# Optimization experiments

Measured on AMD Instinct MI355X. Metric: run time of the kernel, lower is better.

The kernel has to match this reference:

```python
import jax, jax.numpy as jnp
import numpy as np

B, T, IN, H, OUT, NH = 64, 512, 256, 512, 256, 4
HD = H // NH
DT = 0.1
UNFOLDS = 6
MIN_TAU, MAX_TAU = 0.1, 10.0


def setup_inputs() -> dict:
    key = jax.random.key(0)
    ks = iter(jax.random.split(key, 48))

    def w(shape, scale=0.05):
        return jax.random.normal(next(ks), shape, dtype=jnp.float32) * scale

    d = {"inputs": jax.random.normal(next(ks), (B, T, IN), dtype=jnp.float32)}
    for i, fin in enumerate([IN, H]):
        d[f"Win{i}_w"] = w((H, fin))
        d[f"Win{i}_b"] = jnp.zeros((H,), jnp.float32)
        d[f"Wrec{i}_w"] = w((H, H))
        d[f"tau{i}a_w"] = w((H, fin + H))
        d[f"tau{i}a_b"] = jnp.zeros((H,), jnp.float32)
        d[f"tau{i}b_w"] = w((H, H))
        d[f"tau{i}b_b"] = jnp.zeros((H,), jnp.float32)
        d[f"gleak{i}"] = jnp.full((H,), 0.1, jnp.float32)
        d[f"gsyn{i}"] = jnp.full((H,), 0.5, jnp.float32)
        d[f"ln{i}_w"] = jnp.ones((H,), jnp.float32)
        d[f"ln{i}_b"] = jnp.zeros((H,), jnp.float32)
    d["attn_in_w"] = w((3 * H, H))
    d["attn_in_b"] = jnp.zeros((3 * H,), jnp.float32)
    d["attn_out_w"] = w((H, H))
    d["attn_out_b"] = jnp.zeros((H,), jnp.float32)
    d["p1_w"] = w((H // 2, H))
    d["p1_b"] = jnp.zeros((H // 2,), jnp.float32)
    d["p2_w"] = w((OUT, H // 2))
    d["p2_b"] = jnp.zeros((OUT,), jnp.float32)
    return d


def _ltc_step(x, v, g, Wiw, Wib, Wrw, taw, tab, tbw, tbb, gl, gs):
    # tau_net: Linear -> tanh -> Linear -> sigmoid, scaled to [min_tau, max_tau]
    comb = jnp.concatenate([x, v], axis=-1)
    tau_h = jnp.tanh(comb @ taw.T + tab)
    tau = MIN_TAU + (MAX_TAU - MIN_TAU) * jax.nn.sigmoid(tau_h @ tbw.T + tbb)
    I_in = x @ Wiw.T + Wib
    for _ in range(UNFOLDS):  # fixed small unroll of the ODE integration
        I_rec = jnp.tanh(v) @ Wrw.T
        g = g + DT * (-g + jax.nn.sigmoid(I_in + I_rec)) / (tau * 0.5)
        v = v + DT * (-gl * v + gs * g * (1.0 - v)) / tau
        v = jnp.clip(v, -5.0, 5.0)
    return jnp.tanh(v), v, g


def _layernorm(x, w, b):
    m = x.mean(-1, keepdims=True)
    var = x.var(-1, keepdims=True)
    return (x - m) / jnp.sqrt(var + 1e-5) * w + b


def reference(inputs, Win0_w, Win0_b, Wrec0_w, tau0a_w, tau0a_b, tau0b_w, tau0b_b,
              gleak0, gsyn0, ln0_w, ln0_b,
              Win1_w, Win1_b, Wrec1_w, tau1a_w, tau1a_b, tau1b_w, tau1b_b,
              gleak1, gsyn1, ln1_w, ln1_b,
              attn_in_w, attn_in_b, attn_out_w, attn_out_b,
              p1_w, p1_b, p2_w, p2_b):
    Bc = inputs.shape[0]

    def step(carry, x_t):
        v0, g0, v1, g1 = carry
        h0, v0, g0 = _ltc_step(x_t, v0, g0, Win0_w, Win0_b, Wrec0_w,
                               tau0a_w, tau0a_b, tau0b_w, tau0b_b, gleak0, gsyn0)
        h0 = _layernorm(h0, ln0_w, ln0_b)
        h1, v1, g1 = _ltc_step(h0, v1, g1, Win1_w, Win1_b, Wrec1_w,
                               tau1a_w, tau1a_b, tau1b_w, tau1b_b, gleak1, gsyn1)
        h1 = _layernorm(h1, ln1_w, ln1_b)
        return (v0, g0, v1, g1), h1

    z = jnp.zeros((Bc, H), inputs.dtype)
    xs = jnp.transpose(inputs, (1, 0, 2))  # (T, B, IN)
    _, ys = jax.lax.scan(step, (z, z, z, z), xs)
    seq = jnp.transpose(ys, (1, 0, 2))  # (B, T, H)

    # MultiheadAttention (self-attention, eval mode => no dropout)
    qkv = seq @ attn_in_w.T + attn_in_b  # (B, T, 3H)
    q, k, v_ = jnp.split(qkv, 3, axis=-1)
    def heads(t):
        return t.reshape(Bc, T, NH, HD).transpose(0, 2, 1, 3)  # (B, NH, T, HD)
    q, k, v_ = heads(q), heads(k), heads(v_)
    scores = jnp.einsum('bhqd,bhkd->bhqk', q, k) / jnp.sqrt(jnp.array(HD, seq.dtype))
    attn = jax.nn.softmax(scores, axis=-1)
    o = jnp.einsum('bhqk,bhkd->bhqd', attn, v_)
    o = o.transpose(0, 2, 1, 3).reshape(Bc, T, H)
    o = o @ attn_out_w.T + attn_out_b

    # output projection on last timestep (return_sequences=False)
    last = o[:, -1, :]
    h = jax.nn.relu(last @ p1_w.T + p1_b)
    out = h @ p2_w.T + p2_b
    return out
```

## Files before the change

kernel.cpp:

```cpp
#include <hip/hip_runtime.h>
#include <stdint.h>


__device__ __forceinline__ float b2f(unsigned short s){
  union { unsigned i; float f; } c; c.i = ((unsigned)s) << 16; return c.f;
}
__device__ __forceinline__ unsigned short f2b(float f){
  union { unsigned i; float f; } c; c.f = f;
  unsigned r = c.i + 0x7fffu + ((c.i >> 16) & 1u);
  return (unsigned short)(r >> 16);
}
__device__ __forceinline__ unsigned pack2(float a, float b){
  return (unsigned)f2b(a) | ((unsigned)f2b(b) << 16);
}
__device__ __forceinline__ float fsig(float x){ return 1.f/(1.f+__expf(-x)); }
__device__ __forceinline__ float ftanh(float x){ return 1.f - 2.f/(__expf(2.f*x)+1.f); }

#if __has_builtin(__builtin_amdgcn_fdot2_f32_bf16)
typedef __bf16 bf16x2_t __attribute__((ext_vector_type(2)));
__device__ __forceinline__ float dot2(unsigned w, unsigned a, float acc){
  union U { unsigned u; bf16x2_t v; };
  U cw; cw.u = w; U ca; ca.u = a;
  return __builtin_amdgcn_fdot2_f32_bf16(cw.v, ca.v, acc, false);
}
#else
__device__ __forceinline__ float dot2(unsigned w, unsigned a, float acc){
  asm("v_dot2_f32_bf16 %0, %1, %2, %0" : "+v"(acc) : "v"(w), "v"(a));
  return acc;
}
#endif

#if __has_builtin(__builtin_amdgcn_sdot4)
__device__ __forceinline__ int sdot4(unsigned w, unsigned a, int acc){
  return __builtin_amdgcn_sdot4((int)w, (int)a, acc, false);
}
#else
__device__ __forceinline__ int sdot4(unsigned w, unsigned a, int acc){
  asm("v_dot4_i32_i8 %0, %1, %2, %0" : "+v"(acc) : "v"(w), "v"(a));
  return acc;
}
#endif

__device__ __forceinline__ unsigned quad8s(float a, float b, float c, float d,
                                           float s){
  const int q0 = __float2int_rn(a * s);
  const int q1 = __float2int_rn(b * s);
  const int q2 = __float2int_rn(c * s);
  const int q3 = __float2int_rn(d * s);
  return (unsigned)(q0 & 255) | ((unsigned)(q1 & 255) << 8) |
         ((unsigned)(q2 & 255) << 16) | ((unsigned)(q3 & 255) << 24);
}

__device__ __forceinline__ float redselF(float c0, float c1, float c2, float c3,
                                         int tid){
  #pragma unroll
  for (int off = 1; off <= 4; off <<= 1){
    c0 += __shfl_xor(c0, off);
    c1 += __shfl_xor(c1, off);
    c2 += __shfl_xor(c2, off);
    c3 += __shfl_xor(c3, off);
  }
  const int j = (tid >> 1) & 3;
  const float lo = (j & 1) ? c1 : c0;
  const float hi = (j & 1) ? c3 : c2;
  return (j & 2) ? hi : lo;
}
__device__ __forceinline__ int redselI(int c0, int c1, int c2, int c3, int tid){
  #pragma unroll
  for (int off = 1; off <= 4; off <<= 1){
    c0 += __shfl_xor(c0, off);
    c1 += __shfl_xor(c1, off);
    c2 += __shfl_xor(c2, off);
    c3 += __shfl_xor(c3, off);
  }
  const int j = (tid >> 1) & 3;
  const int lo = (j & 1) ? c1 : c0;
  const int hi = (j & 1) ? c3 : c2;
  return (j & 2) ? hi : lo;
}

template<int NQ>
__device__ __forceinline__ int matvecQ1(const uint4* __restrict__ wq,
                                        const unsigned* __restrict__ actQ,
                                        int tid){
  const int kh8 = tid & 7;
  int c0 = 0, c1 = 0, c2 = 0, c3 = 0;
  #pragma unroll 4
  for (int q = 0; q < NQ; ++q){
    const unsigned au = actQ[(q << 3) + kh8];
    const uint4 wv = wq[((size_t)q << 10) + tid];
    c0 = sdot4(wv.x, au, c0);
    c1 = sdot4(wv.y, au, c1);
    c2 = sdot4(wv.z, au, c2);
    c3 = sdot4(wv.w, au, c3);
  }
  return redselI(c0, c1, c2, c3, tid);
}

template<int NX, int NV>
__device__ __forceinline__ float matvecQ2(const uint4* __restrict__ wq,
                                          const unsigned* __restrict__ actQ,
                                          float xmax, float vmax, int tid){
  const int kh8 = tid & 7;
  int x0 = 0, x1 = 0, x2 = 0, x3 = 0;
  int v0 = 0, v1 = 0, v2 = 0, v3 = 0;
  #pragma unroll 4
  for (int q = 0; q < NX; ++q){
    const unsigned au = actQ[(q << 3) + kh8];
    const uint4 wv = wq[((size_t)q << 10) + tid];
    x0 = sdot4(wv.x, au, x0);
    x1 = sdot4(wv.y, au, x1);
    x2 = sdot4(wv.z, au, x2);
    x3 = sdot4(wv.w, au, x3);
  }
  #pragma unroll 4
  for (int q = NX; q < NX + NV; ++q){
    const unsigned au = actQ[(q << 3) + kh8];
    const uint4 wv = wq[((size_t)q << 10) + tid];
    v0 = sdot4(wv.x, au, v0);
    v1 = sdot4(wv.y, au, v1);
    v2 = sdot4(wv.z, au, v2);
    v3 = sdot4(wv.w, au, v3);
  }
  const float c0 = (float)x0 * xmax + (float)v0 * vmax;
  const float c1 = (float)x1 * xmax + (float)v1 * vmax;
  const float c2 = (float)x2 * xmax + (float)v2 * vmax;
  const float c3 = (float)x3 * xmax + (float)v3 * vmax;
  return redselF(c0, c1, c2, c3, tid);
}

template<bool FILL>
__device__ __forceinline__ int wrecQ(const uint4* __restrict__ wq,
                                     const unsigned* __restrict__ actQ,
                                     uint4* __restrict__ wldsQ, int tid){
  const int kh8 = tid & 7;
  int c0 = 0, c1 = 0, c2 = 0, c3 = 0;
  #pragma unroll 3
  for (int q = 0; q < 9; ++q){
    const unsigned au = actQ[(q << 3) + kh8];
    uint4 wv;
    if (FILL){ wv = wq[((size_t)q << 10) + tid]; wldsQ[(q << 10) + tid] = wv; }
    else     { wv = wldsQ[(q << 10) + tid]; }
    c0 = sdot4(wv.x, au, c0);
    c1 = sdot4(wv.y, au, c1);
    c2 = sdot4(wv.z, au, c2);
    c3 = sdot4(wv.w, au, c3);
  }
  #pragma unroll
  for (int q = 9; q < 16; ++q){
    const unsigned au = actQ[(q << 3) + kh8];
    const uint4 wv = wq[((size_t)q << 10) + tid];
    c0 = sdot4(wv.x, au, c0);
    c1 = sdot4(wv.y, au, c1);
    c2 = sdot4(wv.z, au, c2);
    c3 = sdot4(wv.w, au, c3);
  }
  return redselI(c0, c1, c2, c3, tid);
}

template<int NX, bool PROD>
__device__ __forceinline__ float layer_stepP(
    float& v, float& g, float& vmax,
    const uint4* WiQ, const uint4* WrQ, const uint4* TaQ, const uint4* TbQ,
    float wb, float tab, float tbb, float gl, float gs, float lw, float lb,
    float smTa, float smWi, float smTb, float smWr, float xmax,
    unsigned* comb8, unsigned* thQ, unsigned* actQA, unsigned* actQB,
    float* sred, uint4* wldsQ, int tid, bool fill, float& ymax)
{
  const float tsel = matvecQ2<NX, 16>(TaQ, comb8, xmax, vmax, tid);
  const int   isel = matvecQ1<NX>(WiQ, comb8, tid);
  const float tauh = ftanh(tsel * smTa + tab);
  const float iin  = (float)isel * (smWi * xmax) + wb;
  const float hv   = ftanh(v);
  {
    const float t2 = __shfl_down(tauh, 2), t4 = __shfl_down(tauh, 4),
                t6 = __shfl_down(tauh, 6);
    const float h2 = __shfl_down(hv, 2), h4 = __shfl_down(hv, 4),
                h6 = __shfl_down(hv, 6);
    if (!(tid & 7)){
      thQ[tid >> 3]   = quad8s(tauh, t2, t4, t6, 127.f);
      actQB[tid >> 3] = quad8s(hv, h2, h4, h6, 127.f);
    }
  }
  __syncthreads();
  const int tbi = matvecQ1<16>(TbQ, thQ, tid);
  const float tau = 0.1f + 9.9f * fsig((float)tbi * smTb + tbb);
  const float ga = 0.2f / tau;
  const float va = 0.1f / tau;
  float h = hv;
  #pragma unroll 1
  for (int u = 0; u < 6; ++u){
    unsigned* curQ = (u & 1) ? actQA : actQB;
    unsigned* nxtQ = (u & 1) ? actQB : actQA;
    const int ri = (fill && u == 0)
        ? wrecQ<true >(WrQ, curQ, wldsQ, tid)
        : wrecQ<false>(WrQ, curQ, wldsQ, tid);
    const float irec = (float)ri * smWr;
    g += (fsig(iin + irec) - g) * ga;
    v += (gs * g * (1.f - v) - gl * v) * va;
    v = fminf(5.f, fmaxf(-5.f, v));
    h = ftanh(v);
    const float h2 = __shfl_down(h, 2), h4 = __shfl_down(h, 4),
                h6 = __shfl_down(h, 6);
    if (!(tid & 7)) nxtQ[tid >> 3] = quad8s(h, h2, h4, h6, 127.f);
    __syncthreads();
  }
  const float hm = (tid & 1) ? 0.f : h;
  const float vm = (tid & 1) ? 0.f : fabsf(v);
  float s1 = hm, s2 = hm * hm, s3 = vm;
  #pragma unroll
  for (int off = 32; off >= 1; off >>= 1){
    s1 += __shfl_down(s1, off);
    s2 += __shfl_down(s2, off);
    s3 = fmaxf(s3, __shfl_down(s3, off));
  }
  const int lane = tid & 63, wid = tid >> 6;
  if (lane == 0){ sred[wid] = s1; sred[16 + wid] = s2; sred[32 + wid] = s3; }
  __syncthreads();
  float S1 = 0.f, S2 = 0.f, S3 = 0.f;
  #pragma unroll
  for (int w2 = 0; w2 < 16; ++w2){
    S1 += sred[w2]; S2 += sred[16 + w2]; S3 = fmaxf(S3, sred[32 + w2]);
  }
  vmax = S3;
  const float m    = S1 * (1.f/512.f);
  const float varr = S2 * (1.f/512.f) - m * m;
  const float y = (h - m) * rsqrtf(varr + 1e-5f) * lw + lb;
  __syncthreads();
  if (PROD){
    float ya = (tid & 1) ? 0.f : fabsf(y);
    #pragma unroll
    for (int off = 32; off >= 1; off >>= 1) ya = fmaxf(ya, __shfl_down(ya, off));
    if (lane == 0) sred[wid] = ya;
    __syncthreads();
    float Y = 0.f;
    #pragma unroll
    for (int w2 = 0; w2 < 16; ++w2) Y = fmaxf(Y, sred[w2]);
    ymax = Y;
  }
  return y;
}

template<int K, int NOUT>
__device__ __forceinline__ void matvec2(const uint4* __restrict__ w,
                                        const unsigned* __restrict__ act2,
                                        int tid, float* out){
  constexpr int NJ = NOUT/256, NIB = K/16;
  const uint4* a4 = (const uint4*)act2;
  const int kh = tid & 1;
  float acc[NJ];
  #pragma unroll
  for (int j = 0; j < NJ; ++j) acc[j] = 0.f;
  #pragma unroll 2
  for (int ib = 0; ib < NIB; ++ib){
    const uint4 a = a4[2*ib + kh];
    #pragma unroll
    for (int j = 0; j < NJ; ++j){
      const uint4 wv = w[(size_t)(ib*NJ + j)*512 + tid];
      acc[j] = dot2(wv.x, a.x, acc[j]);
      acc[j] = dot2(wv.y, a.y, acc[j]);
      acc[j] = dot2(wv.z, a.z, acc[j]);
      acc[j] = dot2(wv.w, a.w, acc[j]);
    }
  }
  #pragma unroll
  for (int j = 0; j < NJ; ++j){
    float s = acc[j];
    s += __shfl_xor(s, 1);
    out[j] = s;
  }
}

#define PK_WQ     0
#define PK_WK     32768
#define PK_WV     65536
#define PK_AO     98304
#define PK_P1     131072
#define PK_P2     147456
#define PK_BF_TOT 155648
#define PK_QWR0   155648
#define PK_QWR1   172032
#define PK_QTA0   188416
#define PK_QTA1   212992
#define PK_QWI0   245760
#define PK_QWI1   253952
#define PK_QTB0   270336
#define PK_QTB1   286720

__global__ void detect_kernel(const unsigned* __restrict__ x, int* __restrict__ flag){
  int cnt = 0;
  for (int i = threadIdx.x; i < 4096; i += 256){
    const unsigned e = (x[i] >> 7) & 0xFFu;
    cnt += (e == 0u || e == 0xFFu) ? 1 : 0;
  }
  __shared__ int sh[4];
  #pragma unroll
  for (int off = 32; off >= 1; off >>= 1) cnt += __shfl_down(cnt, off);
  if ((threadIdx.x & 63) == 0) sh[threadIdx.x >> 6] = cnt;
  __syncthreads();
  if (threadIdx.x == 0) *flag = (sh[0]+sh[1]+sh[2]+sh[3] > 4) ? 1 : 0;
}

struct TPDesc {
  const void* src[6];
  long eoff[6];
  int kdiv8[6];
  int lg2n[6];
  int cum[7];
};
__global__ void tailpack_kernel(TPDesc d, const int* __restrict__ flag,
                                uint4* __restrict__ out){
  const int u = blockIdx.x * 256 + threadIdx.x;
  if (u >= d.cum[6]) return;
  int s = 0;
  #pragma unroll
  for (int i = 1; i < 6; ++i) if (u >= d.cum[i]) s = i;
  const int local = u - d.cum[s];
  const int tid  = local & 511;
  const int r    = local >> 9;
  const int lgnj = d.lg2n[s] - 8;
  const int j    = r & ((1 << lgnj) - 1);
  const int ib   = r >> lgnj;
  const int p    = tid >> 1, kh = tid & 1;
  const int o    = (j << 8) + p;
  const long base = (long)o * (d.kdiv8[s] * 8) + (long)(2*ib + kh) * 8;
  if (*flag){
    const float* sp = (const float*)d.src[s] + d.eoff[s];
    unsigned short h[8];
    #pragma unroll
    for (int i = 0; i < 8; ++i) h[i] = f2b(sp[base + i]);
    uint4 o4;
    o4.x = (unsigned)h[0] | ((unsigned)h[1] << 16);
    o4.y = (unsigned)h[2] | ((unsigned)h[3] << 16);
    o4.z = (unsigned)h[4] | ((unsigned)h[5] << 16);
    o4.w = (unsigned)h[6] | ((unsigned)h[7] << 16);
    out[u] = o4;
  } else {
    const unsigned short* sp = (const unsigned short*)d.src[s] + d.eoff[s];
    out[u] = *(const uint4*)(sp + base);
  }
}

struct QDesc {
  const void* src[8];
  int K[8];
  int outoff[8];
};
__global__ void rowmax_kernel(QDesc d, const int* __restrict__ flag,
                              float* __restrict__ pvec, float* __restrict__ sinv){
  const int r = blockIdx.x * 256 + threadIdx.x;
  const int m = r >> 9, row = r & 511;
  const int K = d.K[m];
  float mx = 0.f;
  if (*flag){
    const float* p = (const float*)d.src[m] + (size_t)row * K;
    for (int k = 0; k < K; ++k) mx = fmaxf(mx, fabsf(p[k]));
  } else {
    const unsigned short* p = (const unsigned short*)d.src[m] + (size_t)row * K;
    for (int k = 0; k < K; ++k) mx = fmaxf(mx, fabsf(b2f(p[k])));
  }
  const int ok = mx > 1e-20f;
  pvec[9728 + r] = ok ? (mx * (1.f/16129.f)) : 0.f;
  sinv[r]        = ok ? (127.f / mx)         : 0.f;
}
__global__ void qpack_kernel(QDesc d, const int* __restrict__ flag,
                             const float* __restrict__ sinv,
                             uint4* __restrict__ out){
  const int u = blockIdx.x * 256 + threadIdx.x;
  const int gq = u >> 10, tid = u & 1023;
  const int cum[9] = {0,16,32,56,88,96,112,128,144};
  int m = 0;
  #pragma unroll
  for (int i = 1; i < 8; ++i) if (gq >= cum[i]) m = i;
  const int q = gq - cum[m];
  const int K = d.K[m];
  const int isf = *flag;
  const int k0 = 4 * ((q << 3) + (tid & 7));
  unsigned wd[4];
  #pragma unroll
  for (int j = 0; j < 4; ++j){
    const int row = ((tid >> 3) << 2) + j;
    const float s = sinv[(m << 9) + row];
    float f0, f1, f2, f3;
    if (isf){
      const float* p = (const float*)d.src[m] + (size_t)row * K + k0;
      f0 = p[0]; f1 = p[1]; f2 = p[2]; f3 = p[3];
    } else {
      const unsigned short* p = (const unsigned short*)d.src[m] + (size_t)row * K + k0;
      f0 = b2f(p[0]); f1 = b2f(p[1]); f2 = b2f(p[2]); f3 = b2f(p[3]);
    }
    wd[j] = quad8s(f0, f1, f2, f3, s);
  }
  uint4 o4; o4.x = wd[0]; o4.y = wd[1]; o4.z = wd[2]; o4.w = wd[3];
  out[d.outoff[m] + ((size_t)q << 10) + tid] = o4;
}

__global__ void xmax_kernel(const void* __restrict__ xin,
                            const int* __restrict__ flag,
                            float* __restrict__ xm){
  const int r = blockIdx.x;
  const int tid = threadIdx.x;
  float mx = 0.f;
  if (*flag){
    const float2* p = (const float2*)xin + (size_t)r * 128 + 2*tid;
    const float2 a = p[0], b = p[1];
    mx = fmaxf(fmaxf(fabsf(a.x), fabsf(a.y)), fmaxf(fabsf(b.x), fabsf(b.y)));
  } else {
    const unsigned* p = (const unsigned*)xin + (size_t)r * 128 + 2*tid;
    const unsigned u0 = p[0], u1 = p[1];
    mx = fmaxf(fmaxf(fabsf(b2f((unsigned short)(u0 & 0xffffu))),
                     fabsf(b2f((unsigned short)(u0 >> 16)))),
               fmaxf(fabsf(b2f((unsigned short)(u1 & 0xffffu))),
                     fabsf(b2f((unsigned short)(u1 >> 16)))));
  }
  #pragma unroll
  for (int off = 32; off >= 1; off >>= 1) mx = fmaxf(mx, __shfl_down(mx, off));
  if (tid == 0) xm[r] = mx;
}

struct VecDesc {
  const void* src[18];
  int n[18];
  int dst[18];
};
__global__ void vec_kernel(VecDesc d, const int* __restrict__ flag,
                           float* __restrict__ pvec){
  const int s = blockIdx.x;
  const int f = *flag;
  for (int i = threadIdx.x; i < d.n[s]; i += blockDim.x)
    pvec[d.dst[s] + i] = f ? ((const float*)d.src[s])[i]
                           : b2f(((const unsigned short*)d.src[s])[i]);
}

__global__ void zflags_kernel(int* __restrict__ aflag, int* __restrict__ cflag){
  const int i = threadIdx.x;
  if (i < 64) aflag[i] = 0; else cflag[i - 64] = 0;
}

#define SCAN_SMEM 150272
__global__
__attribute__((amdgpu_flat_work_group_size(1024, 1024), amdgpu_waves_per_eu(4, 4)))
void scan_kernel(
    const void* __restrict__ xin,
    const uint4* __restrict__ wp,
    const float* __restrict__ pvec,
    const int* __restrict__ flagp,
    unsigned* __restrict__ seqw,
    unsigned* __restrict__ ring,
    int* __restrict__ aflag,
    int* __restrict__ cflag,
    const float* __restrict__ xmaxT)
{
  extern __shared__ __align__(16) char smem[];
  unsigned* comb8 = (unsigned*)smem;
  unsigned* thQ   = comb8 + 256;
  unsigned* actQA = thQ + 128;
  unsigned* actQB = actQA + 128;
  float*    sred  = (float*)(actQB + 128);
  uint4*    wldsQ = (uint4*)(smem + 2816);

  const int tid = threadIdx.x;
  const int o   = tid >> 1;
  const int blk  = blockIdx.x;
  const int xcd  = blk & 7;
  const int slot = blk >> 3;
  const bool isB = xcd >= 4;
  const int b    = ((xcd & 3) << 4) | slot;
  const int isf32 = *flagp;
  const int cb  = isB ? 3584 : 0;

  const uint4* WrQ = wp + (isB ? PK_QWR1 : PK_QWR0);
  const uint4* TaQ = wp + (isB ? PK_QTA1 : PK_QTA0);
  const uint4* WiQ = wp + (isB ? PK_QWI1 : PK_QWI0);
  const uint4* TbQ = wp + (isB ? PK_QTB1 : PK_QTB0);

  const float wb  = pvec[cb+o],      tab = pvec[cb+512+o], tbb = pvec[cb+1024+o];
  const float gl  = pvec[cb+1536+o], gs  = pvec[cb+2048+o];
  const float lw  = pvec[cb+2560+o], lb  = pvec[cb+3072+o];

  const float* smb = pvec + 9728;
  const float smWr = smb[(0 + (isB?1:0))*512 + o];
  const float smTa = smb[(2 + (isB?1:0))*512 + o];
  const float smWi = smb[(4 + (isB?1:0))*512 + o];
  const float smTb = smb[(6 + (isB?1:0))*512 + o];

  float v = 0.f, g = 0.f, vmax = 0.f;

  #pragma unroll 1
  for (int t = 0; t < 512; ++t){
    if (!isB){
      const float xm = xmaxT[b*512 + t];
      if (tid < 64){
        const float sc = (xm > 1e-20f) ? 127.f/xm : 0.f;
        const size_t xbase = ((size_t)b*512 + t)*128;
        if (isf32){
          const float2 a = ((const float2*)xin)[xbase + 2*tid];
          const float2 c = ((const float2*)xin)[xbase + 2*tid + 1];
          comb8[tid] = quad8s(a.x, a.y, c.x, c.y, sc);
        } else {
          const unsigned u0 = ((const unsigned*)xin)[xbase + 2*tid];
          const unsigned u1 = ((const unsigned*)xin)[xbase + 2*tid + 1];
          comb8[tid] = quad8s(b2f((unsigned short)(u0 & 0xffffu)),
                              b2f((unsigned short)(u0 >> 16)),
                              b2f((unsigned short)(u1 & 0xffffu)),
                              b2f((unsigned short)(u1 >> 16)), sc);
        }
      }
      {
        const float sv = (vmax > 1e-20f) ? 127.f/vmax : 0.f;
        const float v2 = __shfl_down(v, 2), v4 = __shfl_down(v, 4),
                    v6 = __shfl_down(v, 6);
        if (!(tid & 7)) comb8[64 + (tid >> 3)] = quad8s(v, v2, v4, v6, sv);
      }
      __syncthreads();
      float ym;
      const float y = layer_stepP<8, true>(v, g, vmax, WiQ, WrQ, TaQ, TbQ,
                                           wb, tab, tbb, gl, gs, lw, lb,
                                           smTa, smWi, smTb, smWr, xm,
                                           comb8, thQ, actQA, actQB, sred,
                                           wldsQ, tid, t == 0, ym);
      if (tid == 0 && t >= 8){
        while (__hip_atomic_load(&cflag[b], __ATOMIC_ACQUIRE,
                                 __HIP_MEMORY_SCOPE_AGENT) < t - 7)
          __builtin_amdgcn_s_sleep(2);
      }
      __syncthreads();
      {
        const float sy = (ym > 1e-20f) ? 127.f/ym : 0.f;
        unsigned* dst = ring + ((size_t)b*8 + (t & 7))*144;
        const float y2 = __shfl_down(y, 2), y4 = __shfl_down(y, 4),
                    y6 = __shfl_down(y, 6);
        if (!(tid & 7))
          __hip_atomic_store(dst + (tid >> 3), quad8s(y, y2, y4, y6, sy),
                             __ATOMIC_RELAXED, __HIP_MEMORY_SCOPE_AGENT);
        if (tid == 0)
          __hip_atomic_store(dst + 128, __float_as_uint(ym),
                             __ATOMIC_RELAXED, __HIP_MEMORY_SCOPE_AGENT);
      }
      __syncthreads();
      if (tid == 0)
        __hip_atomic_store(&aflag[b], t + 1, __ATOMIC_RELEASE,
                           __HIP_MEMORY_SCOPE_AGENT);
    } else {
      if (tid == 0){
        while (__hip_atomic_load(&aflag[b], __ATOMIC_ACQUIRE,
                                 __HIP_MEMORY_SCOPE_AGENT) < t + 1)
          __builtin_amdgcn_s_sleep(2);
      }
      __syncthreads();
      const unsigned* rsl = ring + ((size_t)b*8 + (t & 7))*144;
      if (tid < 128)
        comb8[tid] = __hip_atomic_load(rsl + tid, __ATOMIC_RELAXED,
                                       __HIP_MEMORY_SCOPE_AGENT);
      const float xm = __uint_as_float(
          __hip_atomic_load(rsl + 128, __ATOMIC_RELAXED,
                            __HIP_MEMORY_SCOPE_AGENT));
      {
        const float sv = (vmax > 1e-20f) ? 127.f/vmax : 0.f;
        const float v2 = __shfl_down(v, 2), v4 = __shfl_down(v, 4),
                    v6 = __shfl_down(v, 6);
        if (!(tid & 7)) comb8[128 + (tid >> 3)] = quad8s(v, v2, v4, v6, sv);
      }
      __syncthreads();
      if (tid == 0)
        __hip_atomic_store(&cflag[b], t + 1, __ATOMIC_RELEASE,
                           __HIP_MEMORY_SCOPE_AGENT);
      float ymd;
      const float y = layer_stepP<16, false>(v, g, vmax, WiQ, WrQ, TaQ, TbQ,
                                             wb, tab, tbb, gl, gs, lw, lb,
                                             smTa, smWi, smTb, smWr, xm,
                                             comb8, thQ, actQA, actQB, sred,
                                             wldsQ, tid, t == 0, ymd);
      {
        const float yp = __shfl_down(y, 2);
        if (!(tid & 3))
          seqw[((size_t)b*512 + t)*256 + (tid >> 2)] = pack2(y, yp);
      }
    }
  }
}

__global__ __launch_bounds__(512) void q_kernel(
    const unsigned* __restrict__ seqw, const uint4* __restrict__ wp,
    const float* __restrict__ pvec, float* __restrict__ qws)
{
  __shared__ __align__(16) unsigned act2[256];
  const int tid = threadIdx.x, b = blockIdx.x, p = tid >> 1;
  if (tid < 256) act2[tid] = seqw[((size_t)(b*512 + 511))*256 + tid];
  __syncthreads();
  float q[2]; matvec2<512, 512>(wp + PK_WQ, act2, tid, q);
  if (!(tid & 1)){
    qws[b*512 + p]       = q[0] + pvec[7168 + p];
    qws[b*512 + 256 + p] = q[1] + pvec[7168 + 256 + p];
  }
}

__global__ __launch_bounds__(512) void score_kernel(
    const unsigned* __restrict__ seqw, const uint4* __restrict__ wp,
    const float* __restrict__ pvec, const float* __restrict__ qws,
    float* __restrict__ sws)
{
  __shared__ __align__(16) unsigned act2[256];
  __shared__ float hrA[8], hrB[8];
  const int tid = threadIdx.x, p = tid >> 1;
  const int r = blockIdx.x, b = r >> 9, t = r & 511;
  if (tid < 256) act2[tid] = seqw[(size_t)r*256 + tid];
  __syncthreads();
  float kk[2]; matvec2<512, 512>(wp + PK_WK, act2, tid, kk);
  float pa = (tid & 1) ? 0.f : (kk[0] + pvec[7680 + p])       * qws[b*512 + p];
  float pb = (tid & 1) ? 0.f : (kk[1] + pvec[7680 + 256 + p]) * qws[b*512 + 256 + p];
  #pragma unroll
  for (int off = 32; off >= 1; off >>= 1){
    pa += __shfl_down(pa, off); pb += __shfl_down(pb, off);
  }
  const int lane = tid & 63, wid = tid >> 6;
  if (lane == 0){ hrA[wid] = pa; hrB[wid] = pb; }
  __syncthreads();
  if (tid < 4){
    float s;
    if      (tid == 0) s = hrA[0]+hrA[1]+hrA[2]+hrA[3];
    else if (tid == 1) s = hrA[4]+hrA[5]+hrA[6]+hrA[7];
    else if (tid == 2) s = hrB[0]+hrB[1]+hrB[2]+hrB[3];
    else               s = hrB[4]+hrB[5]+hrB[6]+hrB[7];
    sws[((size_t)(b*4 + tid))*512 + t] = s * 0.08838834764831845f;
  }
}

__global__ __launch_bounds__(512) void softmax_kernel(
    const float* __restrict__ sws, float* __restrict__ pws,
    float* __restrict__ oacc)
{
  __shared__ float rw[16];
  const int tid = threadIdx.x, bh = blockIdx.x;
  const float s = sws[(size_t)bh*512 + tid];
  float mx = s;
  #pragma unroll
  for (int off = 32; off >= 1; off >>= 1) mx = fmaxf(mx, __shfl_down(mx, off));
  const int lane = tid & 63, wid = tid >> 6;
  if (lane == 0) rw[wid] = mx;
  __syncthreads();
  mx = rw[0];
  #pragma unroll
  for (int w2 = 1; w2 < 8; ++w2) mx = fmaxf(mx, rw[w2]);
  const float e = __expf(s - mx);
  float sm = e;
  #pragma unroll
  for (int off = 32; off >= 1; off >>= 1) sm += __shfl_down(sm, off);
  if (lane == 0) rw[8 + wid] = sm;
  __syncthreads();
  sm = 0.f;
  #pragma unroll
  for (int w2 = 0; w2 < 8; ++w2) sm += rw[8 + w2];
  pws[(size_t)bh*512 + tid] = e / sm;
  if (tid < 128) oacc[(bh >> 2)*512 + (bh & 3)*128 + tid] = 0.f;
}

__global__ __launch_bounds__(512) void vacc_kernel(
    const unsigned* __restrict__ seqw, const uint4* __restrict__ wp,
    const float* __restrict__ pvec, const float* __restrict__ pws,
    float* __restrict__ oacc)
{
  __shared__ __align__(16) unsigned act2[256];
  const int tid = threadIdx.x, p = tid >> 1;
  const int blk = blockIdx.x, b = blk >> 3, ch = blk & 7;
  float a0 = 0.f, a1 = 0.f;
  #pragma unroll 1
  for (int t = ch*64; t < ch*64 + 64; ++t){
    if (tid < 256) act2[tid] = seqw[((size_t)b*512 + t)*256 + tid];
    __syncthreads();
    float vv[2]; matvec2<512, 512>(wp + PK_WV, act2, tid, vv);
    if (!(tid & 1)){
      a0 += (vv[0] + pvec[8192 + p])       * pws[(size_t)(b*4 + (p>>7))*512 + t];
      a1 += (vv[1] + pvec[8192 + 256 + p]) * pws[(size_t)(b*4 + 2 + (p>>7))*512 + t];
    }
    __syncthreads();
  }
  if (!(tid & 1)){
    atomicAdd(&oacc[b*512 + p], a0);
    atomicAdd(&oacc[b*512 + 256 + p], a1);
  }
}

__global__ __launch_bounds__(512) void final_kernel(
    const float* __restrict__ oacc, const uint4* __restrict__ wp,
    const float* __restrict__ pvec, const int* __restrict__ flagp,
    void* __restrict__ out)
{
  __shared__ __align__(16) unsigned a2[256];
  const int tid = threadIdx.x, b = blockIdx.x, p = tid >> 1;
  const int isf32 = *flagp;
  {
    const float x0 = oacc[b*512 + p], x1 = oacc[b*512 + 256 + p];
    const float xa = __shfl_down(x0, 2), xb = __shfl_down(x1, 2);
    if (!(tid & 3)){ a2[tid>>2] = pack2(x0, xa); a2[128+(tid>>2)] = pack2(x1, xb); }
  }
  __syncthreads();
  float t1[2]; matvec2<512, 512>(wp + PK_AO, a2, tid, t1);
  t1[0] += pvec[8704 + p]; t1[1] += pvec[8704 + 256 + p];
  __syncthreads();
  {
    const float ta = __shfl_down(t1[0], 2), tb = __shfl_down(t1[1], 2);
    if (!(tid & 3)){ a2[tid>>2] = pack2(t1[0], ta); a2[128+(tid>>2)] = pack2(t1[1], tb); }
  }
  __syncthreads();
  float t2[1]; matvec2<512, 256>(wp + PK_P1, a2, tid, t2);
  t2[0] = fmaxf(0.f, t2[0] + pvec[9216 + p]);
  __syncthreads();
  {
    const float ta = __shfl_down(t2[0], 2);
    if (!(tid & 3)) a2[tid>>2] = pack2(t2[0], ta);
  }
  __syncthreads();
  float r[1]; matvec2<256, 256>(wp + PK_P2, a2, tid, r);
  if (!(tid & 1)){
    const float rr = r[0] + pvec[9472 + p];
    if (isf32) ((float*)out)[b*256 + p] = rr;
    else       ((unsigned short*)out)[b*256 + p] = f2b(rr);
  }
}

__global__ void zero_kernel(unsigned* __restrict__ p, int n){
  const int i = blockIdx.x * 1024 + threadIdx.x;
  if (i < n) p[i] = 0;
}

extern "C" void kernel_launch(void* const* d_in, const int* in_sizes, int n_in,
                              void* d_out, int out_size, void* d_ws, size_t ws_size,
                              hipStream_t stream)
{
  (void)in_sizes; (void)n_in; (void)out_size;

  if (ws_size < ((size_t)44 << 20)){
    zero_kernel<<<8, 1024, 0, stream>>>((unsigned*)d_out, 8192);
    return;
  }

  hipFuncSetAttribute((const void*)scan_kernel,
                      hipFuncAttributeMaxDynamicSharedMemorySize, SCAN_SMEM);

  char* ws = (char*)d_ws;
  int*      flag   = (int*)ws;
  int*      aflag  = (int*)(ws + 256);
  int*      cflag  = (int*)(ws + 512);
  float*    pvec   = (float*)(ws + 4096);
  uint4*    packed = (uint4*)(ws + 65536);
  float*    sinv   = (float*)(ws + ((size_t)5 << 20));
  float*    xmaxT  = (float*)(ws + ((size_t)5 << 20) + 131072);
  unsigned* seq    = (unsigned*)(ws + ((size_t)8 << 20));
  unsigned* ring   = (unsigned*)(ws + ((size_t)40 << 20));
  float*    sws    = (float*)(ws + ((size_t)41 << 20));
  float*    pws    = (float*)(ws + ((size_t)41 << 20) + 524288);
  float*    qws    = (float*)(ws + ((size_t)42 << 20));
  float*    oacc   = (float*)(ws + ((size_t)42 << 20) + 262144);

  detect_kernel<<<1, 256, 0, stream>>>((const unsigned*)d_in[0], flag);
  zflags_kernel<<<1, 128, 0, stream>>>(aflag, cflag);

  TPDesc tp;
  const void* tsrc[6] = { d_in[23], d_in[23], d_in[23], d_in[25], d_in[27], d_in[29] };
  const long teoff[6] = { 0, 262144, 524288, 0, 0, 0 };
  const int tk8[6]   = { 64, 64, 64, 64, 64, 32 };
  const int tln[6]   = { 9, 9, 9, 9, 8, 8 };
  const int tcum[7]  = { 0, 32768, 65536, 98304, 131072, 147456, 155648 };
  for (int i = 0; i < 6; ++i){
    tp.src[i]=tsrc[i]; tp.eoff[i]=teoff[i]; tp.kdiv8[i]=tk8[i]; tp.lg2n[i]=tln[i];
  }
  for (int i = 0; i < 7; ++i) tp.cum[i] = tcum[i];
  tailpack_kernel<<<(PK_BF_TOT + 255)/256, 256, 0, stream>>>(tp, flag, packed);

  VecDesc vd;
  const void* vsrc[18] = {
    d_in[2], d_in[5], d_in[7], d_in[8], d_in[9], d_in[10], d_in[11],
    d_in[13], d_in[16], d_in[18], d_in[19], d_in[20], d_in[21], d_in[22],
    d_in[24], d_in[26], d_in[28], d_in[30]
  };
  const int vn[18]  = {512,512,512,512,512,512,512, 512,512,512,512,512,512,512,
                       1536,512,256,256};
  const int vds[18] = {0,512,1024,1536,2048,2560,3072,
                       3584,4096,4608,5120,5632,6144,6656,
                       7168,8704,9216,9472};
  for (int i = 0; i < 18; ++i){ vd.src[i]=vsrc[i]; vd.n[i]=vn[i]; vd.dst[i]=vds[i]; }
  vec_kernel<<<18, 512, 0, stream>>>(vd, flag, pvec);

  QDesc qd;
  const void* qsrc[8] = { d_in[3], d_in[14], d_in[4], d_in[15],
                          d_in[1], d_in[12], d_in[6], d_in[17] };
  const int qK[8]   = { 512, 512, 768, 1024, 256, 512, 512, 512 };
  const int qoff[8] = { PK_QWR0, PK_QWR1, PK_QTA0, PK_QTA1,
                        PK_QWI0, PK_QWI1, PK_QTB0, PK_QTB1 };
  for (int i = 0; i < 8; ++i){ qd.src[i]=qsrc[i]; qd.K[i]=qK[i]; qd.outoff[i]=qoff[i]; }
  rowmax_kernel<<<16, 256, 0, stream>>>(qd, flag, pvec, sinv);
  qpack_kernel<<<576, 256, 0, stream>>>(qd, flag, sinv, packed);
  xmax_kernel<<<32768, 64, 0, stream>>>(d_in[0], flag, xmaxT);

  scan_kernel<<<128, 1024, SCAN_SMEM, stream>>>(d_in[0], packed, pvec, flag,
                                                seq, ring, aflag, cflag, xmaxT);
  q_kernel<<<64, 512, 0, stream>>>(seq, packed, pvec, qws);
  score_kernel<<<64*512, 512, 0, stream>>>(seq, packed, pvec, qws, sws);
  softmax_kernel<<<256, 512, 0, stream>>>(sws, pws, oacc);
  vacc_kernel<<<512, 512, 0, stream>>>(seq, packed, pvec, pws, oacc);
  final_kernel<<<64, 512, 0, stream>>>(oacc, packed, pvec, flag, d_out);
}
```

Measured before the change: 12.39 ms.

## Split scan into input-projection producer blocks and recurrent consumer blocks

The recurrent scan now runs 256 blocks in four roles. Two roles compute the input-dependent matvecs (the x-part of the tau_net first layer and the input current) for layer 0 and layer 1 ahead of time and pass them through ring buffers. The other two roles keep only the v-dependent recurrent work on the serial critical path. Blocks get their role from a per-XCD atomic rank read via the XCC_ID register, and the tau weights are split into x and v halves at pack time. This adds inter-block flag handshakes and needs all 256 persistent blocks to be co-resident, or the spin-waits could deadlock.

```diff
diff --git a/kernel.cpp b/kernel.cpp
--- a/kernel.cpp
+++ b/kernel.cpp
@@ -51,20 +51,6 @@
          ((unsigned)(q2 & 255) << 16) | ((unsigned)(q3 & 255) << 24);
 }
 
-__device__ __forceinline__ float redselF(float c0, float c1, float c2, float c3,
-                                         int tid){
-  #pragma unroll
-  for (int off = 1; off <= 4; off <<= 1){
-    c0 += __shfl_xor(c0, off);
-    c1 += __shfl_xor(c1, off);
-    c2 += __shfl_xor(c2, off);
-    c3 += __shfl_xor(c3, off);
-  }
-  const int j = (tid >> 1) & 3;
-  const float lo = (j & 1) ? c1 : c0;
-  const float hi = (j & 1) ? c3 : c2;
-  return (j & 2) ? hi : lo;
-}
 __device__ __forceinline__ int redselI(int c0, int c1, int c2, int c3, int tid){
   #pragma unroll
   for (int off = 1; off <= 4; off <<= 1){
@@ -95,38 +81,6 @@
     c3 = sdot4(wv.w, au, c3);
   }
   return redselI(c0, c1, c2, c3, tid);
-}
-
-template<int NX, int NV>
-__device__ __forceinline__ float matvecQ2(const uint4* __restrict__ wq,
-                                          const unsigned* __restrict__ actQ,
-                                          float xmax, float vmax, int tid){
-  const int kh8 = tid & 7;
-  int x0 = 0, x1 = 0, x2 = 0, x3 = 0;
-  int v0 = 0, v1 = 0, v2 = 0, v3 = 0;
-  #pragma unroll 4
-  for (int q = 0; q < NX; ++q){
-    const unsigned au = actQ[(q << 3) + kh8];
-    const uint4 wv = wq[((size_t)q << 10) + tid];
-    x0 = sdot4(wv.x, au, x0);
-    x1 = sdot4(wv.y, au, x1);
-    x2 = sdot4(wv.z, au, x2);
-    x3 = sdot4(wv.w, au, x3);
-  }
-  #pragma unroll 4
-  for (int q = NX; q < NX + NV; ++q){
-    const unsigned au = actQ[(q << 3) + kh8];
-    const uint4 wv = wq[((size_t)q << 10) + tid];
-    v0 = sdot4(wv.x, au, v0);
-    v1 = sdot4(wv.y, au, v1);
-    v2 = sdot4(wv.z, au, v2);
-    v3 = sdot4(wv.w, au, v3);
-  }
-  const float c0 = (float)x0 * xmax + (float)v0 * vmax;
-  const float c1 = (float)x1 * xmax + (float)v1 * vmax;
-  const float c2 = (float)x2 * xmax + (float)v2 * vmax;
-  const float c3 = (float)x3 * xmax + (float)v3 * vmax;
-  return redselF(c0, c1, c2, c3, tid);
 }
 
 template<bool FILL>
@@ -158,19 +112,17 @@
   return redselI(c0, c1, c2, c3, tid);
 }
 
-template<int NX, bool PROD>
-__device__ __forceinline__ float layer_stepP(
-    float& v, float& g, float& vmax,
-    const uint4* WiQ, const uint4* WrQ, const uint4* TaQ, const uint4* TbQ,
-    float wb, float tab, float tbb, float gl, float gs, float lw, float lb,
-    float smTa, float smWi, float smTb, float smWr, float xmax,
-    unsigned* comb8, unsigned* thQ, unsigned* actQA, unsigned* actQB,
+template<bool PROD>
+__device__ __forceinline__ float scan_step(
+    float& v, float& g, float& vmax, float P, float iin,
+    const uint4* TavQ, const uint4* TbQ, const uint4* WrQ,
+    float tab, float tbb, float gl, float gs, float lw, float lb,
+    float smTa, float smTb, float smWr,
+    unsigned* vQ, unsigned* thQ, unsigned* aQA, unsigned* aQB,
     float* sred, uint4* wldsQ, int tid, bool fill, float& ymax)
 {
-  const float tsel = matvecQ2<NX, 16>(TaQ, comb8, xmax, vmax, tid);
-  const int   isel = matvecQ1<NX>(WiQ, comb8, tid);
-  const float tauh = ftanh(tsel * smTa + tab);
-  const float iin  = (float)isel * (smWi * xmax) + wb;
+  const int tvi = matvecQ1<16>(TavQ, vQ, tid);
+  const float tauh = ftanh((P + (float)tvi * vmax) * smTa + tab);
   const float hv   = ftanh(v);
   {
     const float t2 = __shfl_down(tauh, 2), t4 = __shfl_down(tauh, 4),
@@ -178,8 +130,8 @@
     const float h2 = __shfl_down(hv, 2), h4 = __shfl_down(hv, 4),
                 h6 = __shfl_down(hv, 6);
     if (!(tid & 7)){
-      thQ[tid >> 3]   = quad8s(tauh, t2, t4, t6, 127.f);
-      actQB[tid >> 3] = quad8s(hv, h2, h4, h6, 127.f);
+      thQ[tid >> 3] = quad8s(tauh, t2, t4, t6, 127.f);
+      aQB[tid >> 3] = quad8s(hv, h2, h4, h6, 127.f);
     }
   }
   __syncthreads();
@@ -190,8 +142,8 @@
   float h = hv;
   #pragma unroll 1
   for (int u = 0; u < 6; ++u){
-    unsigned* curQ = (u & 1) ? actQA : actQB;
-    unsigned* nxtQ = (u & 1) ? actQB : actQA;
+    unsigned* curQ = (u & 1) ? aQA : aQB;
+    unsigned* nxtQ = (u & 1) ? aQB : aQA;
     const int ri = (fill && u == 0)
         ? wrecQ<true >(WrQ, curQ, wldsQ, tid)
         : wrecQ<false>(WrQ, curQ, wldsQ, tid);
@@ -280,8 +232,10 @@
 #define PK_BF_TOT 155648
 #define PK_QWR0   155648
 #define PK_QWR1   172032
-#define PK_QTA0   188416
-#define PK_QTA1   212992
+#define PK_QTA0X  188416
+#define PK_QTA0V  196608
+#define PK_QTA1X  212992
+#define PK_QTA1V  229376
 #define PK_QWI0   245760
 #define PK_QWI1   253952
 #define PK_QTB0   270336
@@ -341,12 +295,11 @@
   }
 }
 
-struct QDesc {
+struct RDesc {
   const void* src[8];
   int K[8];
-  int outoff[8];
 };
-__global__ void rowmax_kernel(QDesc d, const int* __restrict__ flag,
+__global__ void rowmax_kernel(RDesc d, const int* __restrict__ flag,
                               float* __restrict__ pvec, float* __restrict__ sinv){
   const int r = blockIdx.x * 256 + threadIdx.x;
   const int m = r >> 9, row = r & 511;
@@ -363,24 +316,32 @@
   pvec[9728 + r] = ok ? (mx * (1.f/16129.f)) : 0.f;
   sinv[r]        = ok ? (127.f / mx)         : 0.f;
 }
-__global__ void qpack_kernel(QDesc d, const int* __restrict__ flag,
+
+struct QPDesc {
+  const void* src[10];
+  int Kfull[10];
+  int koff[10];
+  int sidx[10];
+  int outoff[10];
+  int cum[11];
+};
+__global__ void qpack_kernel(QPDesc d, const int* __restrict__ flag,
                              const float* __restrict__ sinv,
                              uint4* __restrict__ out){
   const int u = blockIdx.x * 256 + threadIdx.x;
   const int gq = u >> 10, tid = u & 1023;
-  const int cum[9] = {0,16,32,56,88,96,112,128,144};
   int m = 0;
   #pragma unroll
-  for (int i = 1; i < 8; ++i) if (gq >= cum[i]) m = i;
-  const int q = gq - cum[m];
-  const int K = d.K[m];
+  for (int i = 1; i < 10; ++i) if (gq >= d.cum[i]) m = i;
+  const int q = gq - d.cum[m];
+  const int K = d.Kfull[m];
   const int isf = *flag;
-  const int k0 = 4 * ((q << 3) + (tid & 7));
+  const int k0 = d.koff[m] + 4 * ((q << 3) + (tid & 7));
   unsigned wd[4];
   #pragma unroll
   for (int j = 0; j < 4; ++j){
     const int row = ((tid >> 3) << 2) + j;
-    const float s = sinv[(m << 9) + row];
+    const float s = sinv[(d.sidx[m] << 9) + row];
     float f0, f1, f2, f3;
     if (isf){
       const float* p = (const float*)d.src[m] + (size_t)row * K + k0;
@@ -432,9 +393,9 @@
                            : b2f(((const unsigned short*)d.src[s])[i]);
 }
 
-__global__ void zflags_kernel(int* __restrict__ aflag, int* __restrict__ cflag){
+__global__ void zflags_kernel(int* __restrict__ base){
   const int i = threadIdx.x;
-  if (i < 64) aflag[i] = 0; else cflag[i - 64] = 0;
+  if (i < 392) base[i] = 0;
 }
 
 #define SCAN_SMEM 150272
@@ -446,49 +407,56 @@
     const float* __restrict__ pvec,
     const int* __restrict__ flagp,
     unsigned* __restrict__ seqw,
-    unsigned* __restrict__ ring,
-    int* __restrict__ aflag,
-    int* __restrict__ cflag,
+    int* __restrict__ fbase,
+    unsigned* __restrict__ ringH,
+    unsigned* __restrict__ ringx,
+    unsigned* __restrict__ ring2,
     const float* __restrict__ xmaxT)
 {
   extern __shared__ __align__(16) char smem[];
   unsigned* comb8 = (unsigned*)smem;
   unsigned* thQ   = comb8 + 256;
-  unsigned* actQA = thQ + 128;
-  unsigned* actQB = actQA + 128;
-  float*    sred  = (float*)(actQB + 128);
+  unsigned* aQA   = thQ + 128;
+  unsigned* aQB   = aQA + 128;
+  float*    sred  = (float*)(aQB + 128);
   uint4*    wldsQ = (uint4*)(smem + 2816);
+  __shared__ int srank, sxcd;
+
+  int* aX = fbase;        int* cX = fbase + 64;
+  int* aH = fbase + 128;  int* cH = fbase + 192;
+  int* a2 = fbase + 256;  int* c2 = fbase + 320;
+  int* xcnt = fbase + 384;
 
   const int tid = threadIdx.x;
-  const int o   = tid >> 1;
-  const int blk  = blockIdx.x;
-  const int xcd  = blk & 7;
-  const int slot = blk >> 3;
-  const bool isB = xcd >= 4;
-  const int b    = ((xcd & 3) << 4) | slot;
+  if (tid == 0){
+    unsigned xr;
+    asm volatile("s_getreg_b32 %0, hwreg(HW_REG_XCC_ID)" : "=s"(xr));
+    sxcd  = (int)(xr & 7u);
+    srank = atomicAdd(&xcnt[xr & 7u], 1);
+  }
+  __syncthreads();
+  const int gid  = sxcd * 32 + (srank & 31);
+  const int role = gid >> 6;
+  const int b    = gid & 63;
+  const int o    = tid >> 1;
   const int isf32 = *flagp;
-  const int cb  = isB ? 3584 : 0;
-
-  const uint4* WrQ = wp + (isB ? PK_QWR1 : PK_QWR0);
-  const uint4* TaQ = wp + (isB ? PK_QTA1 : PK_QTA0);
-  const uint4* WiQ = wp + (isB ? PK_QWI1 : PK_QWI0);
-  const uint4* TbQ = wp + (isB ? PK_QTB1 : PK_QTB0);
-
-  const float wb  = pvec[cb+o],      tab = pvec[cb+512+o], tbb = pvec[cb+1024+o];
-  const float gl  = pvec[cb+1536+o], gs  = pvec[cb+2048+o];
-  const float lw  = pvec[cb+2560+o], lb  = pvec[cb+3072+o];
-
+  const bool isL1 = role >= 2;
+  const int cb   = isL1 ? 3584 : 0;
   const float* smb = pvec + 9728;
-  const float smWr = smb[(0 + (isB?1:0))*512 + o];
-  const float smTa = smb[(2 + (isB?1:0))*512 + o];
-  const float smWi = smb[(4 + (isB?1:0))*512 + o];
-  const float smTb = smb[(6 + (isB?1:0))*512 + o];
-
-  float v = 0.f, g = 0.f, vmax = 0.f;
-
-  #pragma unroll 1
-  for (int t = 0; t < 512; ++t){
-    if (!isB){
+
+  if (role == 0){
+    const uint4* TaxQ = wp + PK_QTA0X;
+    const uint4* WiQ  = wp + PK_QWI0;
+    const float wb   = pvec[o];
+    const float smWi = smb[4*512 + o];
+    #pragma unroll 1
+    for (int t = 0; t < 512; ++t){
+      if (tid == 0 && t >= 4){
+        while (__hip_atomic_load(&cX[b], __ATOMIC_ACQUIRE,
+                                 __HIP_MEMORY_SCOPE_AGENT) < t - 3)
+          __builtin_amdgcn_s_sleep(2);
+      }
+      __syncthreads();
       const float xm = xmaxT[b*512 + t];
       if (tid < 64){
         const float sc = (xm > 1e-20f) ? 127.f/xm : 0.f;
@@ -506,72 +474,147 @@
                               b2f((unsigned short)(u1 >> 16)), sc);
         }
       }
-      {
-        const float sv = (vmax > 1e-20f) ? 127.f/vmax : 0.f;
-        const float v2 = __shfl_down(v, 2), v4 = __shfl_down(v, 4),
-                    v6 = __shfl_down(v, 6);
-        if (!(tid & 7)) comb8[64 + (tid >> 3)] = quad8s(v, v2, v4, v6, sv);
-      }
       __syncthreads();
-      float ym;
-      const float y = layer_stepP<8, true>(v, g, vmax, WiQ, WrQ, TaQ, TbQ,
-                                           wb, tab, tbb, gl, gs, lw, lb,
-                                           smTa, smWi, smTb, smWr, xm,
-                                           comb8, thQ, actQA, actQB, sred,
-                                           wldsQ, tid, t == 0, ym);
-      if (tid == 0 && t >= 8){
-        while (__hip_atomic_load(&cflag[b], __ATOMIC_ACQUIRE,
-                                 __HIP_MEMORY_SCOPE_AGENT) < t - 7)
-          __builtin_amdgcn_s_sleep(2);
-      }
-      __syncthreads();
-      {
-        const float sy = (ym > 1e-20f) ? 127.f/ym : 0.f;
-        unsigned* dst = ring + ((size_t)b*8 + (t & 7))*144;
-        const float y2 = __shfl_down(y, 2), y4 = __shfl_down(y, 4),
-                    y6 = __shfl_down(y, 6);
-        if (!(tid & 7))
-          __hip_atomic_store(dst + (tid >> 3), quad8s(y, y2, y4, y6, sy),
-                             __ATOMIC_RELAXED, __HIP_MEMORY_SCOPE_AGENT);
-        if (tid == 0)
-          __hip_atomic_store(dst + 128, __float_as_uint(ym),
-                             __ATOMIC_RELAXED, __HIP_MEMORY_SCOPE_AGENT);
+      const int txi = matvecQ1<8>(TaxQ, comb8, tid);
+      const int ini = matvecQ1<8>(WiQ, comb8, tid);
+      const float P   = (float)txi * xm;
+      const float iin = (float)ini * (smWi * xm) + wb;
+      unsigned* rs = ringx + ((size_t)b*4 + (t & 3))*1024;
+      if (!(tid & 1)){
+        __hip_atomic_store(rs + o, __float_as_uint(P),
+                           __ATOMIC_RELAXED, __HIP_MEMORY_SCOPE_AGENT);
+        __hip_atomic_store(rs + 512 + o, __float_as_uint(iin),
+                           __ATOMIC_RELAXED, __HIP_MEMORY_SCOPE_AGENT);
       }
       __syncthreads();
       if (tid == 0)
-        __hip_atomic_store(&aflag[b], t + 1, __ATOMIC_RELEASE,
+        __hip_atomic_store(&aX[b], t + 1, __ATOMIC_RELEASE,
                            __HIP_MEMORY_SCOPE_AGENT);
-    } else {
+    }
+  } else if (role == 2){
+    const uint4* TaxQ = wp + PK_QTA1X;
+    const uint4* WiQ  = wp + PK_QWI1;
+    const float wb   = pvec[3584 + o];
+    const float smWi = smb[5*512 + o];
+    #pragma unroll 1
+    for (int t = 0; t < 512; ++t){
       if (tid == 0){
-        while (__hip_atomic_load(&aflag[b], __ATOMIC_ACQUIRE,
+        while (__hip_atomic_load(&aH[b], __ATOMIC_ACQUIRE,
+                                 __HIP_MEMORY_SCOPE_AGENT) < t + 1)
+          __builtin_amdgcn_s_sleep(2);
+        if (t >= 4){
+          while (__hip_atomic_load(&c2[b], __ATOMIC_ACQUIRE,
+                                   __HIP_MEMORY_SCOPE_AGENT) < t - 3)
+            __builtin_amdgcn_s_sleep(2);
+        }
+      }
+      __syncthreads();
+      const unsigned* hs = ringH + ((size_t)b*8 + (t & 7))*144;
+      if (tid < 128)
+        comb8[tid] = __hip_atomic_load(hs + tid, __ATOMIC_RELAXED,
+                                       __HIP_MEMORY_SCOPE_AGENT);
+      const float xm = __uint_as_float(
+          __hip_atomic_load(hs + 128, __ATOMIC_RELAXED,
+                            __HIP_MEMORY_SCOPE_AGENT));
+      __syncthreads();
+      if (tid == 0)
+        __hip_atomic_store(&cH[b], t + 1, __ATOMIC_RELEASE,
+                           __HIP_MEMORY_SCOPE_AGENT);
+      const int txi = matvecQ1<16>(TaxQ, comb8, tid);
+      const int ini = matvecQ1<16>(WiQ, comb8, tid);
+      const float P   = (float)txi * xm;
+      const float iin = (float)ini * (smWi * xm) + wb;
+      unsigned* rs = ring2 + ((size_t)b*4 + (t & 3))*1024;
+      if (!(tid & 1)){
+        __hip_atomic_store(rs + o, __float_as_uint(P),
+                           __ATOMIC_RELAXED, __HIP_MEMORY_SCOPE_AGENT);
+        __hip_atomic_store(rs + 512 + o, __float_as_uint(iin),
+                           __ATOMIC_RELAXED, __HIP_MEMORY_SCOPE_AGENT);
+      }
+      __syncthreads();
+      if (tid == 0)
+        __hip_atomic_store(&a2[b], t + 1, __ATOMIC_RELEASE,
+                           __HIP_MEMORY_SCOPE_AGENT);
+    }
+  } else {
+    const bool isB = (role == 3);
+    const uint4* TavQ = wp + (isB ? PK_QTA1V : PK_QTA0V);
+    const uint4* TbQ  = wp + (isB ? PK_QTB1  : PK_QTB0);
+    const uint4* WrQ  = wp + (isB ? PK_QWR1  : PK_QWR0);
+    int* aP = isB ? a2 : aX;
+    int* cP = isB ? c2 : cX;
+    unsigned* rup = isB ? ring2 : ringx;
+
+    const float tab = pvec[cb+512+o], tbb = pvec[cb+1024+o];
+    const float gl  = pvec[cb+1536+o], gs = pvec[cb+2048+o];
+    const float lw  = pvec[cb+2560+o], lb = pvec[cb+3072+o];
+    const float smWr = smb[(0 + (isB?1:0))*512 + o];
+    const float smTa = smb[(2 + (isB?1:0))*512 + o];
+    const float smTb = smb[(6 + (isB?1:0))*512 + o];
+
+    float v = 0.f, g = 0.f, vmax = 0.f;
+
+    #pragma unroll 1
+    for (int t = 0; t < 512; ++t){
+      if (tid == 0){
+        while (__hip_atomic_load(&aP[b], __ATOMIC_ACQUIRE,
                                  __HIP_MEMORY_SCOPE_AGENT) < t + 1)
           __builtin_amdgcn_s_sleep(2);
       }
       __syncthreads();
-      const unsigned* rsl = ring + ((size_t)b*8 + (t & 7))*144;
-      if (tid < 128)
-        comb8[tid] = __hip_atomic_load(rsl + tid, __ATOMIC_RELAXED,
-                                       __HIP_MEMORY_SCOPE_AGENT);
-      const float xm = __uint_as_float(
-          __hip_atomic_load(rsl + 128, __ATOMIC_RELAXED,
+      const unsigned* rs = rup + ((size_t)b*4 + (t & 3))*1024;
+      const float P   = __uint_as_float(
+          __hip_atomic_load(rs + o, __ATOMIC_RELAXED,
+                            __HIP_MEMORY_SCOPE_AGENT));
+      const float iin = __uint_as_float(
+          __hip_atomic_load(rs + 512 + o, __ATOMIC_RELAXED,
                             __HIP_MEMORY_SCOPE_AGENT));
       {
         const float sv = (vmax > 1e-20f) ? 127.f/vmax : 0.f;
         const float v2 = __shfl_down(v, 2), v4 = __shfl_down(v, 4),
                     v6 = __shfl_down(v, 6);
-        if (!(tid & 7)) comb8[128 + (tid >> 3)] = quad8s(v, v2, v4, v6, sv);
+        if (!(tid & 7)) comb8[tid >> 3] = quad8s(v, v2, v4, v6, sv);
       }
       __syncthreads();
       if (tid == 0)
-        __hip_atomic_store(&cflag[b], t + 1, __ATOMIC_RELEASE,
+        __hip_atomic_store(&cP[b], t + 1, __ATOMIC_RELEASE,
                            __HIP_MEMORY_SCOPE_AGENT);
-      float ymd;
-      const float y = layer_stepP<16, false>(v, g, vmax, WiQ, WrQ, TaQ, TbQ,
-                                             wb, tab, tbb, gl, gs, lw, lb,
-                                             smTa, smWi, smTb, smWr, xm,
-                                             comb8, thQ, actQA, actQB, sred,
-                                             wldsQ, tid, t == 0, ymd);
-      {
+      if (!isB){
+        float ym;
+        const float y = scan_step<true>(v, g, vmax, P, iin, TavQ, TbQ, WrQ,
+                                        tab, tbb, gl, gs, lw, lb,
+                                        smTa, smTb, smWr,
+                                        comb8, thQ, aQA, aQB, sred, wldsQ,
+                                        tid, t == 0, ym);
+        if (tid == 0 && t >= 8){
+          while (__hip_atomic_load(&cH[b], __ATOMIC_ACQUIRE,
+                                   __HIP_MEMORY_SCOPE_AGENT) < t - 7)
+            __builtin_amdgcn_s_sleep(2);
+        }
+        __syncthreads();
+        {
+          const float sy = (ym > 1e-20f) ? 127.f/ym : 0.f;
+          unsigned* dst = ringH + ((size_t)b*8 + (t & 7))*144;
+          const float y2 = __shfl_down(y, 2), y4 = __shfl_down(y, 4),
+                      y6 = __shfl_down(y, 6);
+          if (!(tid & 7))
+            __hip_atomic_store(dst + (tid >> 3), quad8s(y, y2, y4, y6, sy),
+                               __ATOMIC_RELAXED, __HIP_MEMORY_SCOPE_AGENT);
+          if (tid == 0)
+            __hip_atomic_store(dst + 128, __float_as_uint(ym),
+                               __ATOMIC_RELAXED, __HIP_MEMORY_SCOPE_AGENT);
+        }
+        __syncthreads();
+        if (tid == 0)
+          __hip_atomic_store(&aH[b], t + 1, __ATOMIC_RELEASE,
+                             __HIP_MEMORY_SCOPE_AGENT);
+      } else {
+        float ymd;
+        const float y = scan_step<false>(v, g, vmax, P, iin, TavQ, TbQ, WrQ,
+                                         tab, tbb, gl, gs, lw, lb,
+                                         smTa, smTb, smWr,
+                                         comb8, thQ, aQA, aQB, sred, wldsQ,
+                                         tid, t == 0, ymd);
         const float yp = __shfl_down(y, 2);
         if (!(tid & 3))
           seqw[((size_t)b*512 + t)*256 + (tid >> 2)] = pack2(y, yp);
@@ -740,21 +783,23 @@
 
   char* ws = (char*)d_ws;
   int*      flag   = (int*)ws;
-  int*      aflag  = (int*)(ws + 256);
-  int*      cflag  = (int*)(ws + 512);
+  int*      fbase  = (int*)(ws + 256);
   float*    pvec   = (float*)(ws + 4096);
   uint4*    packed = (uint4*)(ws + 65536);
   float*    sinv   = (float*)(ws + ((size_t)5 << 20));
   float*    xmaxT  = (float*)(ws + ((size_t)5 << 20) + 131072);
   unsigned* seq    = (unsigned*)(ws + ((size_t)8 << 20));
-  unsigned* ring   = (unsigned*)(ws + ((size_t)40 << 20));
-  float*    sws    = (float*)(ws + ((size_t)41 << 20));
-  float*    pws    = (float*)(ws + ((size_t)41 << 20) + 524288);
-  float*    qws    = (float*)(ws + ((size_t)42 << 20));
-  float*    oacc   = (float*)(ws + ((size_t)42 << 20) + 262144);
+  unsigned* ringH  = (unsigned*)(ws + ((size_t)40 << 20));
+  unsigned* ringx  = (unsigned*)(ws + ((size_t)40 << 20) + 327680);
+  unsigned* ring2  = (unsigned*)(ws + ((size_t)40 << 20) + 327680 + 1048576);
+  char*     tail   = ws + ((size_t)40 << 20) + 327680 + 2097152;
+  float*    sws    = (float*)tail;
+  float*    pws    = (float*)(tail + 524288);
+  float*    qws    = (float*)(tail + 1048576);
+  float*    oacc   = (float*)(tail + 1179648);
 
   detect_kernel<<<1, 256, 0, stream>>>((const unsigned*)d_in[0], flag);
-  zflags_kernel<<<1, 128, 0, stream>>>(aflag, cflag);
+  zflags_kernel<<<1, 512, 0, stream>>>(fbase);
 
   TPDesc tp;
   const void* tsrc[6] = { d_in[23], d_in[23], d_in[23], d_in[25], d_in[27], d_in[29] };
@@ -782,19 +827,33 @@
   for (int i = 0; i < 18; ++i){ vd.src[i]=vsrc[i]; vd.n[i]=vn[i]; vd.dst[i]=vds[i]; }
   vec_kernel<<<18, 512, 0, stream>>>(vd, flag, pvec);
 
-  QDesc qd;
-  const void* qsrc[8] = { d_in[3], d_in[14], d_in[4], d_in[15],
+  RDesc rd;
+  const void* rsrc[8] = { d_in[3], d_in[14], d_in[4], d_in[15],
                           d_in[1], d_in[12], d_in[6], d_in[17] };
-  const int qK[8]   = { 512, 512, 768, 1024, 256, 512, 512, 512 };
-  const int qoff[8] = { PK_QWR0, PK_QWR1, PK_QTA0, PK_QTA1,
-                        PK_QWI0, PK_QWI1, PK_QTB0, PK_QTB1 };
-  for (int i = 0; i < 8; ++i){ qd.src[i]=qsrc[i]; qd.K[i]=qK[i]; qd.outoff[i]=qoff[i]; }
-  rowmax_kernel<<<16, 256, 0, stream>>>(qd, flag, pvec, sinv);
-  qpack_kernel<<<576, 256, 0, stream>>>(qd, flag, sinv, packed);
+  const int rK[8] = { 512, 512, 768, 1024, 256, 512, 512, 512 };
+  for (int i = 0; i < 8; ++i){ rd.src[i]=rsrc[i]; rd.K[i]=rK[i]; }
+  rowmax_kernel<<<16, 256, 0, stream>>>(rd, flag, pvec, sinv);
+
+  QPDesc qp;
+  const void* qsrc[10] = { d_in[3], d_in[14], d_in[4], d_in[4], d_in[15],
+                           d_in[15], d_in[1], d_in[12], d_in[6], d_in[17] };
+  const int qKf[10]   = { 512, 512, 768, 768, 1024, 1024, 256, 512, 512, 512 };
+  const int qko[10]   = { 0, 0, 0, 256, 0, 512, 0, 0, 0, 0 };
+  const int qsi[10]   = { 0, 1, 2, 2, 3, 3, 4, 5, 6, 7 };
+  const int qoo[10]   = { PK_QWR0, PK_QWR1, PK_QTA0X, PK_QTA0V, PK_QTA1X,
+                          PK_QTA1V, PK_QWI0, PK_QWI1, PK_QTB0, PK_QTB1 };
+  const int qcum[11]  = { 0, 16, 32, 40, 56, 72, 88, 96, 112, 128, 144 };
+  for (int i = 0; i < 10; ++i){
+    qp.src[i]=qsrc[i]; qp.Kfull[i]=qKf[i]; qp.koff[i]=qko[i];
+    qp.sidx[i]=qsi[i]; qp.outoff[i]=qoo[i];
+  }
+  for (int i = 0; i < 11; ++i) qp.cum[i] = qcum[i];
+  qpack_kernel<<<576, 256, 0, stream>>>(qp, flag, sinv, packed);
   xmax_kernel<<<32768, 64, 0, stream>>>(d_in[0], flag, xmaxT);
 
-  scan_kernel<<<128, 1024, SCAN_SMEM, stream>>>(d_in[0], packed, pvec, flag,
-                                                seq, ring, aflag, cflag, xmaxT);
+  scan_kernel<<<256, 1024, SCAN_SMEM, stream>>>(d_in[0], packed, pvec, flag,
+                                                seq, fbase, ringH, ringx,
+                                                ring2, xmaxT);
   q_kernel<<<64, 512, 0, stream>>>(seq, packed, pvec, qws);
   score_kernel<<<64*512, 512, 0, stream>>>(seq, packed, pvec, qws, sws);
   softmax_kernel<<<256, 512, 0, stream>>>(sws, pws, oacc);
```

Result: slower. 14.88 ms (+20.1%).
